# Kernel tuning notes

Measured on AMD Instinct MI355X. Metric: run time of the kernel, lower is better.

The kernel has to match this reference:

```python
import jax, jax.numpy as jnp
import numpy as np

HID = 16  # module-level output_size constant
D = 64    # input_dim
K = 32    # number of classes / outer nets
B = 8192  # batch


def setup_inputs() -> dict:
    key = jax.random.key(0)
    ks = jax.random.split(key, 9)
    s = 0.1
    return {
        "x": jax.random.normal(ks[0], (B, D), dtype=jnp.float32),
        # inner nets: one tiny 1->16->1 MLP per (k, i)
        "iw1": jax.random.normal(ks[1], (K, D, HID), dtype=jnp.float32) * s,  # Linear(1,16) weight
        "ib1": jax.random.normal(ks[2], (K, D, HID), dtype=jnp.float32) * s,  # Linear(1,16) bias
        "iw2": jax.random.normal(ks[3], (K, D, HID), dtype=jnp.float32) * s,  # Linear(16,1) weight
        "ib2": jax.random.normal(ks[4], (K, D), dtype=jnp.float32) * s,       # Linear(16,1) bias
        # outer nets: one 1->16->1 MLP per k
        "ow1": jax.random.normal(ks[5], (K, HID), dtype=jnp.float32) * s,
        "ob1": jax.random.normal(ks[6], (K, HID), dtype=jnp.float32) * s,
        "ow2": jax.random.normal(ks[7], (K, HID), dtype=jnp.float32) * s,
        "ob2": jax.random.normal(ks[8], (K,), dtype=jnp.float32) * s,
    }


def reference(x, iw1, ib1, iw2, ib2, ow1, ob1, ow2, ob2):
    # Inner nets, all K*D at once. Linear(1,HID) on scalar xi is an outer product.
    # h: [B, K, D, HID]
    h = jax.nn.relu(x[:, None, :, None] * iw1[None] + ib1[None])
    # Linear(HID,1): contract HID -> yi: [B, K, D]
    yi = jnp.einsum('bkdh,kdh->bkd', h, iw2) + ib2[None]
    # sum over input features i -> [B, K]
    sk = yi.sum(axis=2)
    # Outer nets: scalar -> HID -> scalar per k
    g = jax.nn.relu(sk[:, :, None] * ow1[None] + ob1[None])  # [B, K, HID]
    out = jnp.einsum('bkh,kh->bk', g, ow2) + ob2[None]       # [B, K]
    return out
```

## Files before the change

kernel.cpp:

```cpp
#include <hip/hip_runtime.h>
#include <hip/hip_bf16.h>

#define HID 16
#define DIN 64
#define NK  32
#define NB  8192

typedef float v2f __attribute__((ext_vector_type(2)));
typedef float v4f __attribute__((ext_vector_type(4)));

struct W {
    v2f w1[8], b1[8], w2[8];
};

__device__ __forceinline__ float relu_dot(const W& w, float xd) {
    const v2f xx = {xd, xd};
    v2f acc0 = {0.f, 0.f}, acc1 = {0.f, 0.f};
    #pragma unroll
    for (int hp = 0; hp < 8; hp += 2) {
        v2f t0 = __builtin_elementwise_fma(xx, w.w1[hp],     w.b1[hp]);
        v2f t1 = __builtin_elementwise_fma(xx, w.w1[hp + 1], w.b1[hp + 1]);
        t0 = __builtin_elementwise_max(t0, (v2f){0.f, 0.f});
        t1 = __builtin_elementwise_max(t1, (v2f){0.f, 0.f});
        acc0 = __builtin_elementwise_fma(t0, w.w2[hp],     acc0);
        acc1 = __builtin_elementwise_fma(t1, w.w2[hp + 1], acc1);
    }
    const v2f a = acc0 + acc1;
    return a.x + a.y;
}

template<int LVL, class F>
__device__ __forceinline__ float subtree(int j0, int lane, const F& body) {
    if constexpr (LVL == 0) {
        return body(j0);
    } else {
        const float A = subtree<LVL - 1>(j0, lane, body);
        const float B = subtree<LVL - 1>(j0 + (1 << (LVL - 1)), lane, body);
        const int m = 64 >> LVL;
        const bool hi = (lane & m) != 0;
        const float send = hi ? A : B;
        const float recv = __shfl_xor(send, m, 64);
        const float keep = hi ? B : A;
        return keep + recv;
    }
}

__global__ __launch_bounds__(256, 4) void kan_kernel(
    const float* __restrict__ x,
    const float* __restrict__ iw1, const float* __restrict__ ib1,
    const float* __restrict__ iw2, const float* __restrict__ ib2,
    const float* __restrict__ ow1, const float* __restrict__ ob1,
    const float* __restrict__ ow2, const float* __restrict__ ob2,
    float* __restrict__ out)
{
    const int k     = blockIdx.x & (NK - 1);
    const int chunk = blockIdx.x >> 5;
    const int t     = threadIdx.x;
    const int lane  = t & 63;
    const int wid   = t >> 6;
    const int base  = chunk * 256 + wid * 64;

    W w;
    {
        const v4f* p1 = (const v4f*)(iw1 + (k * DIN + lane) * HID);
        const v4f* p2 = (const v4f*)(ib1 + (k * DIN + lane) * HID);
        const v4f* p3 = (const v4f*)(iw2 + (k * DIN + lane) * HID);
        #pragma unroll
        for (int q = 0; q < 4; ++q) {
            ((v4f*)w.w1)[q] = p1[q];
            ((v4f*)w.b1)[q] = p2[q];
            ((v4f*)w.w2)[q] = p3[q];
        }
    }

    float ck = ib2[k * DIN + lane];
    #pragma unroll
    for (int m = 32; m; m >>= 1) ck += __shfl_xor(ck, m, 64);

    const float* __restrict__ xp = x + base * DIN + lane;
    auto body = [&](int j) { return relu_dot(w, xp[j * DIN]); };

    const float sk = subtree<6>(0, lane, body) + ck;

    float o = ob2[k];
    #pragma unroll
    for (int h = 0; h < HID; ++h) {
        const float g = fmaxf(fmaf(sk, ow1[k * HID + h], ob1[k * HID + h]), 0.f);
        o = fmaf(g, ow2[k * HID + h], o);
    }

    const int brev = (int)(__builtin_bitreverse32((unsigned)lane) >> 26);
    out[(base + brev) * NK + k] = o;
}

extern "C" void kernel_launch(void* const* d_in, const int* in_sizes, int n_in,
                              void* d_out, int out_size, void* d_ws, size_t ws_size,
                              hipStream_t stream) {
    const float* x   = (const float*)d_in[0];
    const float* iw1 = (const float*)d_in[1];
    const float* ib1 = (const float*)d_in[2];
    const float* iw2 = (const float*)d_in[3];
    const float* ib2 = (const float*)d_in[4];
    const float* ow1 = (const float*)d_in[5];
    const float* ob1 = (const float*)d_in[6];
    const float* ow2 = (const float*)d_in[7];
    const float* ob2 = (const float*)d_in[8];
    float* out = (float*)d_out;

    const int grid = (NB / 256) * NK;
    kan_kernel<<<grid, 256, 0, stream>>>(x, iw1, ib1, iw2, ib2,
                                         ow1, ob1, ow2, ob2, out);
}
```

Measured before the change: 32.22 us.

## Replace shuffle butterfly reduction tree with per-wave LDS transpose reduction

The recursive shuffle-based butterfly, which reduced the 64 per-batch inner-net results across lanes, is replaced. Each wave now writes its per-feature results into a padded per-wave LDS tile, one pass of 16 batch rows at a time. It then reads them back transposed and finishes with two cross-lane shuffles. The aim is to cut the large number of cross-lane permute operations, at the cost of LDS traffic, about 17 KB of shared memory per block, and relying on intra-wave ordering with no explicit barrier. The output indexing changes from bit-reversed lanes to a direct lane mapping to match the new reduction layout.

```diff
diff --git a/kernel.cpp b/kernel.cpp
--- a/kernel.cpp
+++ b/kernel.cpp
@@ -29,22 +29,6 @@
     return a.x + a.y;
 }
 
-template<int LVL, class F>
-__device__ __forceinline__ float subtree(int j0, int lane, const F& body) {
-    if constexpr (LVL == 0) {
-        return body(j0);
-    } else {
-        const float A = subtree<LVL - 1>(j0, lane, body);
-        const float B = subtree<LVL - 1>(j0 + (1 << (LVL - 1)), lane, body);
-        const int m = 64 >> LVL;
-        const bool hi = (lane & m) != 0;
-        const float send = hi ? A : B;
-        const float recv = __shfl_xor(send, m, 64);
-        const float keep = hi ? B : A;
-        return keep + recv;
-    }
-}
-
 __global__ __launch_bounds__(256, 4) void kan_kernel(
     const float* __restrict__ x,
     const float* __restrict__ iw1, const float* __restrict__ ib1,
@@ -53,12 +37,13 @@
     const float* __restrict__ ow2, const float* __restrict__ ob2,
     float* __restrict__ out)
 {
-    const int k     = blockIdx.x & (NK - 1);
-    const int chunk = blockIdx.x >> 5;
-    const int t     = threadIdx.x;
-    const int lane  = t & 63;
-    const int wid   = t >> 6;
-    const int base  = chunk * 256 + wid * 64;
+    __shared__ float lds[4][DIN * 17];
+
+    const int t    = threadIdx.x;
+    const int lane = t & 63;
+    const int wid  = t >> 6;
+    const int k    = blockIdx.x & (NK - 1);
+    const int base = ((blockIdx.x >> 5) * 4 + wid) * 64;
 
     W w;
     {
@@ -77,10 +62,35 @@
     #pragma unroll
     for (int m = 32; m; m >>= 1) ck += __shfl_xor(ck, m, 64);
 
+    float* __restrict__ myLds = lds[wid];
     const float* __restrict__ xp = x + base * DIN + lane;
-    auto body = [&](int j) { return relu_dot(w, xp[j * DIN]); };
 
-    const float sk = subtree<6>(0, lane, body) + ck;
+    const int jj = lane & 15;
+    const int p  = lane >> 4;
+
+    float rsum[4];
+
+    #pragma unroll
+    for (int pass = 0; pass < 4; ++pass) {
+        const float* __restrict__ xq = xp + pass * 16 * DIN;
+        #pragma unroll
+        for (int j = 0; j < 16; ++j) {
+            myLds[lane * 17 + j] = relu_dot(w, xq[j * DIN]);
+        }
+        __builtin_amdgcn_sched_barrier(0);
+        float s = 0.f;
+        #pragma unroll
+        for (int i = 0; i < 16; ++i) {
+            s += myLds[(p * 16 + i) * 17 + jj];
+        }
+        __builtin_amdgcn_sched_barrier(0);
+        s += __shfl_xor(s, 16, 64);
+        s += __shfl_xor(s, 32, 64);
+        rsum[pass] = s + ck;
+    }
+
+    const float sk = (lane & 32) ? ((lane & 16) ? rsum[3] : rsum[2])
+                                 : ((lane & 16) ? rsum[1] : rsum[0]);
 
     float o = ob2[k];
     #pragma unroll
@@ -89,8 +99,7 @@
         o = fmaf(g, ow2[k * HID + h], o);
     }
 
-    const int brev = (int)(__builtin_bitreverse32((unsigned)lane) >> 26);
-    out[(base + brev) * NK + k] = o;
+    out[(base + lane) * NK + k] = o;
 }
 
 extern "C" void kernel_launch(void* const* d_in, const int* in_sizes, int n_in,
```

Result: faster. 26.49 us (-17.8%).
